# Kernel tuning notes

Measured on AMD Instinct MI355X. Metric: run time of the kernel, lower is better.

Reference implementation:

```python
import jax, jax.numpy as jnp
import numpy as np

B, N, S, VOCAB, D, NNZ = 16, 2048, 4096, 50257, 128, 1048576


def setup_inputs() -> dict:
    key = jax.random.key(0)
    k1, k2, k3, k4, k5, k6 = jax.random.split(key, 6)
    return {
        "subnode_ids": jax.random.randint(k1, (B, S), 0, VOCAB),
        "mask_batch": jax.random.randint(k2, (NNZ,), 0, B),
        "mask_node": jax.random.randint(k3, (NNZ,), 0, N),
        "mask_subnode": jax.random.randint(k4, (NNZ,), 0, S),
        "mask_values": jax.random.uniform(k5, (NNZ,), dtype=jnp.float32),
        "emb_table": jax.random.normal(k6, (VOCAB, D), dtype=jnp.float32),
    }


def reference(subnode_ids, mask_batch, mask_node, mask_subnode, mask_values, emb_table):
    # Gather token embeddings for every (batch, subnode) slot: [B, S, D] -> [B*S, D]
    subnode_emb = emb_table[subnode_ids].reshape(B * S, D)
    # Flattened COO indices (same as batch*max_nodes + node, batch*max_subnodes + subnode)
    row = mask_batch * N + mask_node      # destination node slot in [0, B*N)
    col = mask_batch * S + mask_subnode   # source subnode slot in [0, B*S)
    # Fused gather + weighted scatter-add (== sparse.mm of expanded_mask @ subnode_emb)
    contrib = subnode_emb[col] * mask_values[:, None]           # [NNZ, D]
    pooled = jax.ops.segment_sum(contrib, row, num_segments=B * N)  # [B*N, D]
    return pooled.reshape(B, N, D)
```

## Files before the change

### kernel.cpp

```cpp
#include <hip/hip_runtime.h>
#include <hip/hip_fp16.h>

#define Bq 16
#define Nq 2048
#define Sq 4096
#define Dq 128
#define VOCABq 50257
#define NNZq 1048576
#define ROWS (Bq * Nq)
#define NBIN 2048
#define RPB 16
#define BCAP 768
#define OVF_MAX 65536
#define BTPB 1024
#define BEPT 4

typedef unsigned long long u64;
typedef float vfloat4 __attribute__((ext_vector_type(4)));
typedef unsigned short vushort4 __attribute__((ext_vector_type(4)));
typedef unsigned short vushort8 __attribute__((ext_vector_type(8)));

__global__ __launch_bounds__(256) void cast_kernel(
    const float* __restrict__ emb, unsigned short* __restrict__ emb16)
{
    const int NQUAD = (VOCABq * Dq) / 4;
    int i = blockIdx.x * 256 + threadIdx.x;
    if (i >= NQUAD) return;
    vfloat4 f = reinterpret_cast<const vfloat4*>(emb)[i];
    vushort4 h;
    h.x = __half_as_ushort(__float2half_rn(f.x));
    h.y = __half_as_ushort(__float2half_rn(f.y));
    h.z = __half_as_ushort(__float2half_rn(f.z));
    h.w = __half_as_ushort(__float2half_rn(f.w));
    __builtin_nontemporal_store(h, reinterpret_cast<vushort4*>(emb16) + i);
}

__global__ __launch_bounds__(BTPB) void bin_kernel(
    const int* __restrict__ subnode_ids,
    const int* __restrict__ mb,
    const int* __restrict__ mn,
    const int* __restrict__ ms,
    const float* __restrict__ mv,
    int* __restrict__ binCnt,
    u64* __restrict__ binMem,
    int* __restrict__ ovfn,
    int* __restrict__ ovf)
{
    __shared__ int hist[NBIN];
    __shared__ int base[NBIN];
    int t = threadIdx.x;
    for (int g = t; g < NBIN; g += BTPB) hist[g] = 0;
    __syncthreads();

    int blockBase = blockIdx.x * (BTPB * BEPT);
    int g[BEPT], rank[BEPT];
    u64 pk[BEPT];
    #pragma unroll
    for (int k = 0; k < BEPT; k++) {
        int i   = blockBase + k * BTPB + t;
        int b   = mb[i];
        int row = b * Nq + mn[i];
        int tok = subnode_ids[b * Sq + ms[i]];
        float v = mv[i];
        g[k]  = row >> 4;
        pk[k] = ((u64)(unsigned)__float_as_int(v) << 32)
              | ((u64)(row & 15) << 16)
              | (unsigned)tok;
        rank[k] = atomicAdd(&hist[g[k]], 1);
    }
    __syncthreads();
    for (int gg = t; gg < NBIN; gg += BTPB) {
        int h = hist[gg];
        base[gg] = h ? atomicAdd(&binCnt[gg], h) : 0;
    }
    __syncthreads();
    #pragma unroll
    for (int k = 0; k < BEPT; k++) {
        int p = base[g[k]] + rank[k];
        if (p < BCAP) {
            binMem[(size_t)g[k] * BCAP + p] = pk[k];
        } else {
            int o = atomicAdd(ovfn, 1);
            if (o < OVF_MAX) ovf[o] = blockBase + k * BTPB + t;
        }
    }
}

__global__ __launch_bounds__(256) void pool_kernel(
    const unsigned short* __restrict__ emb16,
    const int* __restrict__ binCnt,
    const u64* __restrict__ binMem,
    float* __restrict__ out)
{
    __shared__ u64 ebuf[BCAP];
    __shared__ int hist[64];
    __shared__ int start[65];
    __shared__ int cursor[64];

    int t   = threadIdx.x;
    int bin = blockIdx.x;
    if (t < 64) hist[t] = 0;
    __syncthreads();

    int n = min(binCnt[bin], BCAP);
    const u64* bm = binMem + (size_t)bin * BCAP;

    u64 myPk[3];
    int myKey[3], myCnt = 0;
    for (int e = t; e < n; e += 256) {
        u64 pk  = bm[e];
        int tok = (int)(pk & 0xFFFF);
        int key = ((tok >> 14) << 4) | (int)((pk >> 16) & 15);
        myPk[myCnt] = pk; myKey[myCnt] = key; myCnt++;
        atomicAdd(&hist[key], 1);
    }
    __syncthreads();
    if (t < 64) {
        int v = hist[t];
        #pragma unroll
        for (int d = 1; d < 64; d <<= 1) {
            int w = __shfl_up(v, d, 64);
            if (t >= d) v += w;
        }
        start[t + 1] = v;
        if (t == 0) start[0] = 0;
    }
    __syncthreads();
    if (t < 64) cursor[t] = start[t];
    __syncthreads();
    for (int k = 0; k < myCnt; k++) {
        int p = atomicAdd(&cursor[myKey[k]], 1);
        ebuf[p] = myPk[k];
    }
    __syncthreads();

    int g    = t >> 4;
    int lane = t & 15;
    vfloat4 a0 = {0.f, 0.f, 0.f, 0.f};
    vfloat4 a1 = {0.f, 0.f, 0.f, 0.f};
    #pragma unroll
    for (int q = 0; q < 4; q++) {
        int s0 = start[q * 16 + g], s1 = start[q * 16 + g + 1];
        int k = s0;
        for (; k + 8 <= s1; k += 8) {
            int   tk[8];
            float vv[8];
            #pragma unroll
            for (int u = 0; u < 8; u++) {
                u64 pk = ebuf[k + u];
                tk[u] = (int)(pk & 0xFFFF);
                vv[u] = __int_as_float((int)(pk >> 32));
            }
            vushort8 e[8];
            #pragma unroll
            for (int u = 0; u < 8; u++)
                e[u] = reinterpret_cast<const vushort8*>(emb16 + (size_t)tk[u] * Dq)[lane];
            #pragma unroll
            for (int u = 0; u < 8; u++) {
                a0.x += __half2float(__ushort_as_half(e[u][0])) * vv[u];
                a0.y += __half2float(__ushort_as_half(e[u][1])) * vv[u];
                a0.z += __half2float(__ushort_as_half(e[u][2])) * vv[u];
                a0.w += __half2float(__ushort_as_half(e[u][3])) * vv[u];
                a1.x += __half2float(__ushort_as_half(e[u][4])) * vv[u];
                a1.y += __half2float(__ushort_as_half(e[u][5])) * vv[u];
                a1.z += __half2float(__ushort_as_half(e[u][6])) * vv[u];
                a1.w += __half2float(__ushort_as_half(e[u][7])) * vv[u];
            }
        }
        for (; k < s1; k++) {
            u64 pk = ebuf[k];
            int   tok = (int)(pk & 0xFFFF);
            float v   = __int_as_float((int)(pk >> 32));
            vushort8 e = reinterpret_cast<const vushort8*>(emb16 + (size_t)tok * Dq)[lane];
            a0.x += __half2float(__ushort_as_half(e[0])) * v;
            a0.y += __half2float(__ushort_as_half(e[1])) * v;
            a0.z += __half2float(__ushort_as_half(e[2])) * v;
            a0.w += __half2float(__ushort_as_half(e[3])) * v;
            a1.x += __half2float(__ushort_as_half(e[4])) * v;
            a1.y += __half2float(__ushort_as_half(e[5])) * v;
            a1.z += __half2float(__ushort_as_half(e[6])) * v;
            a1.w += __half2float(__ushort_as_half(e[7])) * v;
        }
    }
    float* orow = out + ((size_t)bin * RPB + g) * Dq + lane * 8;
    __builtin_nontemporal_store(a0, reinterpret_cast<vfloat4*>(orow));
    __builtin_nontemporal_store(a1, reinterpret_cast<vfloat4*>(orow) + 1);
}

__global__ __launch_bounds__(256) void overflow_kernel(
    const int* __restrict__ subnode_ids,
    const int* __restrict__ mb, const int* __restrict__ mn,
    const int* __restrict__ ms, const float* __restrict__ mv,
    const float* __restrict__ emb,
    const int* __restrict__ ovfn, const int* __restrict__ ovf,
    float* __restrict__ out)
{
    int nov = min(*ovfn, OVF_MAX);
    for (int e = blockIdx.x * 256 + threadIdx.x; e < nov; e += gridDim.x * 256) {
        int i = ovf[e];
        int b = mb[i];
        int row = b * Nq + mn[i];
        int tok = subnode_ids[b * Sq + ms[i]];
        float v = mv[i];
        const float* src = emb + (size_t)tok * Dq;
        float* dst = out + (size_t)row * Dq;
        for (int d = 0; d < Dq; d++) unsafeAtomicAdd(dst + d, src[d] * v);
    }
}

extern "C" void kernel_launch(void* const* d_in, const int* in_sizes, int n_in,
                              void* d_out, int out_size, void* d_ws, size_t ws_size,
                              hipStream_t stream) {
    const int*   subnode_ids  = (const int*)d_in[0];
    const int*   mask_batch   = (const int*)d_in[1];
    const int*   mask_node    = (const int*)d_in[2];
    const int*   mask_subnode = (const int*)d_in[3];
    const float* mask_values  = (const float*)d_in[4];
    const float* emb_table    = (const float*)d_in[5];
    float*       out          = (float*)d_out;

    unsigned short* emb16 = (unsigned short*)d_ws;
    u64* binMem = (u64*)(emb16 + (size_t)VOCABq * Dq + 64 );
    int* binCnt = (int*)(binMem + (size_t)NBIN * BCAP);
    int* ovfn   = binCnt + NBIN;
    int* ovf    = ovfn + 64;

    (void)hipMemsetAsync(binCnt, 0, (NBIN + 64) * sizeof(int), stream);

    const int NQUAD = (VOCABq * Dq) / 4;
    cast_kernel<<<(NQUAD + 255) / 256, 256, 0, stream>>>(emb_table, emb16);
    bin_kernel<<<NNZq / (BTPB * BEPT), BTPB, 0, stream>>>(
        subnode_ids, mask_batch, mask_node, mask_subnode, mask_values,
        binCnt, binMem, ovfn, ovf);
    pool_kernel<<<NBIN, 256, 0, stream>>>(emb16, binCnt, binMem, out);
    overflow_kernel<<<32, 256, 0, stream>>>(
        subnode_ids, mask_batch, mask_node, mask_subnode, mask_values,
        emb_table, ovfn, ovf, out);
}
```

Measured before the change: 137.7 us.

## Fuse cast into bin kernel and fold overflow handling into pool kernel

Merges the fp32-to-fp16 embedding cast into the binning launch as extra blocks so the two independent jobs run concurrently in one launch. The separate overflow kernel is removed; each pool block now scans the overflow list and adds any matching entries for its own rows, so global float atomics are no longer needed. It also pads the per-bin counters to separate cache lines to reduce atomic contention and uses nontemporal loads for streamed COO and bin data. The trade-off is that every pool block walks the whole overflow list serially, which is cheap only while overflow stays rare.

```diff
diff --git a/kernel.cpp b/kernel.cpp
--- a/kernel.cpp
+++ b/kernel.cpp
@@ -14,28 +14,18 @@
 #define OVF_MAX 65536
 #define BTPB 1024
 #define BEPT 4
+#define NBBIN 256
+#define CAST_QPT 4
+#define CSTRIDE 16
 
 typedef unsigned long long u64;
 typedef float vfloat4 __attribute__((ext_vector_type(4)));
 typedef unsigned short vushort4 __attribute__((ext_vector_type(4)));
 typedef unsigned short vushort8 __attribute__((ext_vector_type(8)));
 
-__global__ __launch_bounds__(256) void cast_kernel(
-    const float* __restrict__ emb, unsigned short* __restrict__ emb16)
-{
-    const int NQUAD = (VOCABq * Dq) / 4;
-    int i = blockIdx.x * 256 + threadIdx.x;
-    if (i >= NQUAD) return;
-    vfloat4 f = reinterpret_cast<const vfloat4*>(emb)[i];
-    vushort4 h;
-    h.x = __half_as_ushort(__float2half_rn(f.x));
-    h.y = __half_as_ushort(__float2half_rn(f.y));
-    h.z = __half_as_ushort(__float2half_rn(f.z));
-    h.w = __half_as_ushort(__float2half_rn(f.w));
-    __builtin_nontemporal_store(h, reinterpret_cast<vushort4*>(emb16) + i);
-}
-
-__global__ __launch_bounds__(BTPB) void bin_kernel(
+__global__ __launch_bounds__(BTPB) void cast_bin_kernel(
+    const float* __restrict__ emb,
+    unsigned short* __restrict__ emb16,
     const int* __restrict__ subnode_ids,
     const int* __restrict__ mb,
     const int* __restrict__ mn,
@@ -49,6 +39,26 @@
     __shared__ int hist[NBIN];
     __shared__ int base[NBIN];
     int t = threadIdx.x;
+
+    if (blockIdx.x >= NBBIN) {
+        const int NQUAD = (VOCABq * Dq) / 4;
+        int b0 = (blockIdx.x - NBBIN) * (BTPB * CAST_QPT) + t;
+        #pragma unroll
+        for (int k = 0; k < CAST_QPT; k++) {
+            int i = b0 + k * BTPB;
+            if (i < NQUAD) {
+                vfloat4 f = reinterpret_cast<const vfloat4*>(emb)[i];
+                vushort4 h;
+                h.x = __half_as_ushort(__float2half_rn(f.x));
+                h.y = __half_as_ushort(__float2half_rn(f.y));
+                h.z = __half_as_ushort(__float2half_rn(f.z));
+                h.w = __half_as_ushort(__float2half_rn(f.w));
+                __builtin_nontemporal_store(h, reinterpret_cast<vushort4*>(emb16) + i);
+            }
+        }
+        return;
+    }
+
     for (int g = t; g < NBIN; g += BTPB) hist[g] = 0;
     __syncthreads();
 
@@ -58,10 +68,11 @@
     #pragma unroll
     for (int k = 0; k < BEPT; k++) {
         int i   = blockBase + k * BTPB + t;
-        int b   = mb[i];
-        int row = b * Nq + mn[i];
-        int tok = subnode_ids[b * Sq + ms[i]];
-        float v = mv[i];
+        int b   = __builtin_nontemporal_load(mb + i);
+        int row = b * Nq + __builtin_nontemporal_load(mn + i);
+        int s   = __builtin_nontemporal_load(ms + i);
+        float v = __builtin_nontemporal_load(mv + i);
+        int tok = subnode_ids[b * Sq + s];
         g[k]  = row >> 4;
         pk[k] = ((u64)(unsigned)__float_as_int(v) << 32)
               | ((u64)(row & 15) << 16)
@@ -71,7 +82,7 @@
     __syncthreads();
     for (int gg = t; gg < NBIN; gg += BTPB) {
         int h = hist[gg];
-        base[gg] = h ? atomicAdd(&binCnt[gg], h) : 0;
+        base[gg] = h ? atomicAdd(&binCnt[gg * CSTRIDE], h) : 0;
     }
     __syncthreads();
     #pragma unroll
@@ -90,6 +101,10 @@
     const unsigned short* __restrict__ emb16,
     const int* __restrict__ binCnt,
     const u64* __restrict__ binMem,
+    const int* __restrict__ subnode_ids,
+    const int* __restrict__ mb, const int* __restrict__ mn,
+    const int* __restrict__ ms, const float* __restrict__ mv,
+    const int* __restrict__ ovfn, const int* __restrict__ ovf,
     float* __restrict__ out)
 {
     __shared__ u64 ebuf[BCAP];
@@ -102,13 +117,13 @@
     if (t < 64) hist[t] = 0;
     __syncthreads();
 
-    int n = min(binCnt[bin], BCAP);
+    int n = min(binCnt[bin * CSTRIDE], BCAP);
     const u64* bm = binMem + (size_t)bin * BCAP;
 
     u64 myPk[3];
     int myKey[3], myCnt = 0;
     for (int e = t; e < n; e += 256) {
-        u64 pk  = bm[e];
+        u64 pk  = __builtin_nontemporal_load(bm + e);
         int tok = (int)(pk & 0xFFFF);
         int key = ((tok >> 14) << 4) | (int)((pk >> 16) & 15);
         myPk[myCnt] = pk; myKey[myCnt] = key; myCnt++;
@@ -182,30 +197,29 @@
             a1.w += __half2float(__ushort_as_half(e[7])) * v;
         }
     }
+
+    int nov = min(*ovfn, OVF_MAX);
+    for (int e2 = 0; e2 < nov; e2++) {
+        int i = ovf[e2];
+        int b = mb[i];
+        int row = b * Nq + mn[i];
+        if ((row >> 4) != bin || (row & 15) != g) continue;
+        int tok = subnode_ids[b * Sq + ms[i]];
+        float v = mv[i];
+        vushort8 e = reinterpret_cast<const vushort8*>(emb16 + (size_t)tok * Dq)[lane];
+        a0.x += __half2float(__ushort_as_half(e[0])) * v;
+        a0.y += __half2float(__ushort_as_half(e[1])) * v;
+        a0.z += __half2float(__ushort_as_half(e[2])) * v;
+        a0.w += __half2float(__ushort_as_half(e[3])) * v;
+        a1.x += __half2float(__ushort_as_half(e[4])) * v;
+        a1.y += __half2float(__ushort_as_half(e[5])) * v;
+        a1.z += __half2float(__ushort_as_half(e[6])) * v;
+        a1.w += __half2float(__ushort_as_half(e[7])) * v;
+    }
+
     float* orow = out + ((size_t)bin * RPB + g) * Dq + lane * 8;
     __builtin_nontemporal_store(a0, reinterpret_cast<vfloat4*>(orow));
     __builtin_nontemporal_store(a1, reinterpret_cast<vfloat4*>(orow) + 1);
-}
-
-__global__ __launch_bounds__(256) void overflow_kernel(
-    const int* __restrict__ subnode_ids,
-    const int* __restrict__ mb, const int* __restrict__ mn,
-    const int* __restrict__ ms, const float* __restrict__ mv,
-    const float* __restrict__ emb,
-    const int* __restrict__ ovfn, const int* __restrict__ ovf,
-    float* __restrict__ out)
-{
-    int nov = min(*ovfn, OVF_MAX);
-    for (int e = blockIdx.x * 256 + threadIdx.x; e < nov; e += gridDim.x * 256) {
-        int i = ovf[e];
-        int b = mb[i];
-        int row = b * Nq + mn[i];
-        int tok = subnode_ids[b * Sq + ms[i]];
-        float v = mv[i];
-        const float* src = emb + (size_t)tok * Dq;
-        float* dst = out + (size_t)row * Dq;
-        for (int d = 0; d < Dq; d++) unsafeAtomicAdd(dst + d, src[d] * v);
-    }
 }
 
 extern "C" void kernel_launch(void* const* d_in, const int* in_sizes, int n_in,
@@ -222,18 +236,17 @@
     unsigned short* emb16 = (unsigned short*)d_ws;
     u64* binMem = (u64*)(emb16 + (size_t)VOCABq * Dq + 64 );
     int* binCnt = (int*)(binMem + (size_t)NBIN * BCAP);
-    int* ovfn   = binCnt + NBIN;
+    int* ovfn   = binCnt + NBIN * CSTRIDE;
     int* ovf    = ovfn + 64;
 
-    (void)hipMemsetAsync(binCnt, 0, (NBIN + 64) * sizeof(int), stream);
+    (void)hipMemsetAsync(binCnt, 0, (NBIN * CSTRIDE + 64) * sizeof(int), stream);
 
     const int NQUAD = (VOCABq * Dq) / 4;
-    cast_kernel<<<(NQUAD + 255) / 256, 256, 0, stream>>>(emb_table, emb16);
-    bin_kernel<<<NNZq / (BTPB * BEPT), BTPB, 0, stream>>>(
-        subnode_ids, mask_batch, mask_node, mask_subnode, mask_values,
-        binCnt, binMem, ovfn, ovf);
-    pool_kernel<<<NBIN, 256, 0, stream>>>(emb16, binCnt, binMem, out);
-    overflow_kernel<<<32, 256, 0, stream>>>(
-        subnode_ids, mask_batch, mask_node, mask_subnode, mask_values,
-        emb_table, ovfn, ovf, out);
+    const int NBCAST = (NQUAD + BTPB * CAST_QPT - 1) / (BTPB * CAST_QPT);
+    cast_bin_kernel<<<NBBIN + NBCAST, BTPB, 0, stream>>>(
+        emb_table, emb16, subnode_ids, mask_batch, mask_node, mask_subnode,
+        mask_values, binCnt, binMem, ovfn, ovf);
+    pool_kernel<<<NBIN, 256, 0, stream>>>(
+        emb16, binCnt, binMem, subnode_ids, mask_batch, mask_node, mask_subnode,
+        mask_values, ovfn, ovf, out);
 }
```

Measured after the change: 148.2 us. +7.6%, slower.
